# Kernel optimization log

Measured on AMD Instinct MI355X. Metric: run time of the kernel, lower is better.

## Reference

```python
import jax, jax.numpy as jnp
import numpy as np

EPS = 1e-6

def rmsnorm(x, w):
    v = jnp.mean(jnp.square(x), axis=-1, keepdims=True)
    return x * jax.lax.rsqrt(v + EPS) * w

def setup_inputs() -> dict:
    key = jax.random.key(0)
    ks = jax.random.split(key, 12)
    H, Di, L = 2048, 4096, 1024   # hidden, mamba inner (expand*H), seq tokens
    DT, N, K = 128, 16, 4         # dt_rank, d_state, d_conv
    F = 8192                      # MLP intermediate
    s = lambda k, shp, sc: jax.random.normal(k, shp, jnp.float32) * sc
    return dict(
        hidden_states=s(ks[0], (L, H), 1.0),
        in_ln_w=jnp.ones((H,), jnp.float32),
        pre_ff_ln_w=jnp.ones((H,), jnp.float32),
        in_proj_w=s(ks[1], (2 * Di, H), 0.02),
        conv_w=s(ks[2], (Di, K), 0.1),
        conv_b=s(ks[3], (Di,), 0.1),
        x_proj_w=s(ks[4], (DT + 2 * N, Di), 0.02),
        dt_ln_w=jnp.ones((DT,), jnp.float32),
        b_ln_w=jnp.ones((N,), jnp.float32),
        c_ln_w=jnp.ones((N,), jnp.float32),
        dt_proj_w=s(ks[5], (Di, DT), 0.02),
        dt_proj_b=s(ks[6], (Di,), 0.1),
        A=-jnp.exp(jax.random.uniform(ks[7], (Di, N), jnp.float32, -4.0, 0.0)),
        D=jnp.ones((Di,), jnp.float32),
        out_proj_w=s(ks[8], (H, Di), 0.02),
        gate_up_w=s(ks[9], (2 * F, H), 0.02),
        down_w=s(ks[10], (H, F), 0.02),
    )

def reference(hidden_states, in_ln_w, pre_ff_ln_w, in_proj_w, conv_w, conv_b,
              x_proj_w, dt_ln_w, b_ln_w, c_ln_w, dt_proj_w, dt_proj_b,
              A, D, out_proj_w, gate_up_w, down_w):
    residual = hidden_states
    x = rmsnorm(hidden_states, in_ln_w)
    # --- Mamba mixer (prefill / selective_scan path) ---
    proj = x @ in_proj_w.T                          # [L, 2*Di]
    Di = in_proj_w.shape[0] // 2
    h, gate = proj[:, :Di], proj[:, Di:]
    # causal depthwise conv1d, kernel K, left pad K-1, then silu
    K = conv_w.shape[1]
    L = h.shape[0]
    hp = jnp.pad(h, ((K - 1, 0), (0, 0)))           # [L+K-1, Di]
    idx = jnp.arange(L)[:, None] + jnp.arange(K)[None, :]
    h = jnp.einsum('lkd,dk->ld', hp[idx], conv_w) + conv_b
    h = jax.nn.silu(h)
    # ssm parameters
    ssm = h @ x_proj_w.T                            # [L, DT+2N]
    DTr = dt_ln_w.shape[0]
    N = b_ln_w.shape[0]
    dt = rmsnorm(ssm[:, :DTr], dt_ln_w)
    B = rmsnorm(ssm[:, DTr:DTr + N], b_ln_w)
    C = rmsnorm(ssm[:, DTr + N:], c_ln_w)
    delta = jax.nn.softplus(dt @ dt_proj_w.T + dt_proj_b)   # [L, Di]
    # selective scan (discretize then linear recurrence over L)
    dA = jnp.exp(delta[:, :, None] * A[None, :, :])         # [L, Di, N]
    dBu = delta[:, :, None] * B[:, None, :] * h[:, :, None] # [L, Di, N]
    def step(s, inp):
        da, dbu = inp
        s = da * s + dbu
        return s, s
    s0 = jnp.zeros((Di, N), jnp.float32)
    _, states = jax.lax.scan(step, s0, (dA, dBu))           # [L, Di, N]
    y = jnp.einsum('ldn,ln->ld', states, C) + h * D
    y = y * jax.nn.silu(gate)
    mixer_out = y @ out_proj_w.T                    # [L, H]
    # --- residual + pre-FF norm + gated MLP ---
    residual = residual + mixer_out
    x = rmsnorm(residual, pre_ff_ln_w)
    gu = x @ gate_up_w.T                            # [L, 2F]
    F = down_w.shape[1]
    x = jax.nn.silu(gu[:, :F]) * gu[:, F:]
    ff = x @ down_w.T
    return residual + ff
```

## Files before the change

kernel.cpp:

```cpp
#include <hip/hip_runtime.h>
#include <math.h>

typedef unsigned short u16;
typedef __bf16 bf16x8 __attribute__((ext_vector_type(8)));
typedef short s16x8 __attribute__((ext_vector_type(8)));
typedef short s16x4 __attribute__((ext_vector_type(4)));
typedef float f32x4 __attribute__((ext_vector_type(4)));

__device__ __forceinline__ u16 f2bf(float f) {
  union { float f; unsigned u; } v; v.f = f;
  unsigned u = v.u;
  unsigned r = u + 0x7fffu + ((u >> 16) & 1u);
  return (u16)(r >> 16);
}
__device__ __forceinline__ float bf2f(u16 h) {
  union { unsigned u; float f; } v; v.u = ((unsigned)h) << 16;
  return v.f;
}
__device__ __forceinline__ float fast_softplus(float x) {
  return (x > 20.f) ? x : __logf(1.f + __expf(x));
}
__device__ __forceinline__ float fast_sig(float x) {
  return __builtin_amdgcn_rcpf(1.f + __expf(-x));
}

__device__ __forceinline__ void gld_lds16(const u16* g, u16* l) {
  __builtin_amdgcn_global_load_lds(
      (const __attribute__((address_space(1))) unsigned int*)g,
      (__attribute__((address_space(3))) unsigned int*)l, 16, 0, 0);
}

__global__ __launch_bounds__(256)
void f32_to_bf16_k(const float* __restrict__ src, u16* __restrict__ dst,
                   int n, int n_valid) {
  int i = (blockIdx.x * 256 + threadIdx.x) * 4;
  if (i >= n) return;
  s16x4 o;
  if (i + 3 < n_valid) {
    float4 v = *(const float4*)(src + i);
    o[0] = (short)f2bf(v.x); o[1] = (short)f2bf(v.y);
    o[2] = (short)f2bf(v.z); o[3] = (short)f2bf(v.w);
  } else {
    o[0] = 0; o[1] = 0; o[2] = 0; o[3] = 0;
  }
  *(s16x4*)(dst + i) = o;
}

template <int BN, int MODE>
__global__ __launch_bounds__(256)
void gemm2(const u16* __restrict__ A, const u16* __restrict__ B,
           float* __restrict__ C, u16* __restrict__ Cb,
           const u16* __restrict__ aux, int M, int Nc, int K) {
  constexpr int NJ = BN / 32;
  constexpr int BISS = BN / 32;
  __shared__ __align__(16) u16 As[64 * 64];
  __shared__ __align__(16) u16 Bs[BN * 64];
  const int tid = threadIdx.x;
  const int tm0 = blockIdx.y * 64;
  const int tn0 = blockIdx.x * BN;
  const int wave = tid >> 6;
  const int lane = tid & 63;
  const int wm = (wave >> 1) * 32;
  const int wn = (wave & 1) * (BN / 2);
  const int frow = lane & 15;
  const int fc = lane >> 4;
  const int rmask = frow & 7;

  const int r0 = tid >> 3;
  const int csw = (((tid & 7) ^ (r0 & 7)) << 3);
  const u16* gA = A + (size_t)(tm0 + r0) * K + csw;
  const u16* gB = B + (size_t)(tn0 + r0) * K + csw;
  u16* lA = &As[tid * 8];
  u16* lB = &Bs[tid * 8];

  f32x4 acc[2][NJ];
  f32x4 zero = {0.f, 0.f, 0.f, 0.f};
#pragma unroll
  for (int i = 0; i < 2; ++i)
#pragma unroll
    for (int j = 0; j < NJ; ++j) acc[i][j] = zero;

  for (int kt = 0; kt < K; kt += 64) {
    __syncthreads();
    gld_lds16(gA, lA);
    gld_lds16(gA + (size_t)32 * K, lA + 2048);
#pragma unroll
    for (int b = 0; b < BISS; ++b)
      gld_lds16(gB + (size_t)32 * b * K, lB + b * 2048);
    gA += 64; gB += 64;
    __syncthreads();
#pragma unroll
    for (int s = 0; s < 2; ++s) {
      bf16x8 af[2], bfr[NJ];
#pragma unroll
      for (int i = 0; i < 2; ++i) {
        int addr = (wm + i * 16 + frow) * 64 + (((s * 4 + fc) ^ rmask) << 3);
        af[i] = __builtin_bit_cast(bf16x8, *(const s16x8*)&As[addr]);
      }
#pragma unroll
      for (int j = 0; j < NJ; ++j) {
        int addr = (wn + j * 16 + frow) * 64 + (((s * 4 + fc) ^ rmask) << 3);
        bfr[j] = __builtin_bit_cast(bf16x8, *(const s16x8*)&Bs[addr]);
      }
#pragma unroll
      for (int i = 0; i < 2; ++i)
#pragma unroll
        for (int j = 0; j < NJ; ++j)
          acc[i][j] = __builtin_amdgcn_mfma_f32_16x16x32_bf16(af[i], bfr[j], acc[i][j], 0, 0, 0);
    }
  }
  const int ccol = lane & 15;
  const int crow = (lane >> 4) * 4;
#pragma unroll
  for (int i = 0; i < 2; ++i) {
#pragma unroll
    for (int j = 0; j < NJ; ++j) {
      int gn = tn0 + wn + j * 16 + ccol;
      if (gn < Nc) {
        size_t base = (size_t)(tm0 + wm + i * 16 + crow) * Nc + gn;
#pragma unroll
        for (int r = 0; r < 4; ++r) {
          float c = acc[i][j][r];
          size_t idx = base + (size_t)r * Nc;
          if (MODE == 0) {
            C[idx] = c;
          } else if (MODE == 1) {
            Cb[idx] = f2bf(c * fast_sig(c));
          } else {
            Cb[idx] = f2bf(c * bf2f(aux[idx]));
          }
        }
      }
    }
  }
}

__device__ inline float block_reduce_sum_256(float v) {
  __shared__ float red[4];
  int lane = threadIdx.x & 63, wave = threadIdx.x >> 6;
#pragma unroll
  for (int m = 32; m > 0; m >>= 1) v += __shfl_xor(v, m, 64);
  if (lane == 0) red[wave] = v;
  __syncthreads();
  return red[0] + red[1] + red[2] + red[3];
}

__global__ __launch_bounds__(256)
void rmsnorm2048_k(const float* __restrict__ x, const float* __restrict__ w,
                   u16* __restrict__ y) {
  const int C = 2048;
  const int row = blockIdx.x;
  const int t = threadIdx.x;
  const float4* xr = (const float4*)(x + (size_t)row * C);
  float4 v0 = xr[t];
  float4 v1 = xr[t + 256];
  float ss = v0.x * v0.x + v0.y * v0.y + v0.z * v0.z + v0.w * v0.w +
             v1.x * v1.x + v1.y * v1.y + v1.z * v1.z + v1.w * v1.w;
  float tot = block_reduce_sum_256(ss);
  float sc = rsqrtf(tot * (1.0f / C) + 1e-6f);
  const float4* wr = (const float4*)w;
  float4 w0 = wr[t], w1 = wr[t + 256];
  u16* yr = y + (size_t)row * C;
  s16x4 o0, o1;
  o0[0] = (short)f2bf(v0.x * sc * w0.x); o0[1] = (short)f2bf(v0.y * sc * w0.y);
  o0[2] = (short)f2bf(v0.z * sc * w0.z); o0[3] = (short)f2bf(v0.w * sc * w0.w);
  o1[0] = (short)f2bf(v1.x * sc * w1.x); o1[1] = (short)f2bf(v1.y * sc * w1.y);
  o1[2] = (short)f2bf(v1.z * sc * w1.z); o1[3] = (short)f2bf(v1.w * sc * w1.w);
  *(s16x4*)(yr + t * 4) = o0;
  *(s16x4*)(yr + 1024 + t * 4) = o1;
}

__global__ __launch_bounds__(256)
void add_rmsnorm_k(const float* __restrict__ a, const float* __restrict__ b,
                   const float* __restrict__ w, float* __restrict__ resid,
                   u16* __restrict__ y) {
  const int C = 2048;
  const int row = blockIdx.x;
  const int t = threadIdx.x;
  const float4* ar = (const float4*)(a + (size_t)row * C);
  const float4* br = (const float4*)(b + (size_t)row * C);
  float4 v0 = ar[t], v1 = ar[t + 256];
  float4 u0 = br[t], u1 = br[t + 256];
  v0.x += u0.x; v0.y += u0.y; v0.z += u0.z; v0.w += u0.w;
  v1.x += u1.x; v1.y += u1.y; v1.z += u1.z; v1.w += u1.w;
  float4* rr = (float4*)(resid + (size_t)row * C);
  rr[t] = v0; rr[t + 256] = v1;
  float ss = v0.x * v0.x + v0.y * v0.y + v0.z * v0.z + v0.w * v0.w +
             v1.x * v1.x + v1.y * v1.y + v1.z * v1.z + v1.w * v1.w;
  float tot = block_reduce_sum_256(ss);
  float sc = rsqrtf(tot * (1.0f / C) + 1e-6f);
  const float4* wr = (const float4*)w;
  float4 w0 = wr[t], w1 = wr[t + 256];
  u16* yr = y + (size_t)row * C;
  s16x4 o0, o1;
  o0[0] = (short)f2bf(v0.x * sc * w0.x); o0[1] = (short)f2bf(v0.y * sc * w0.y);
  o0[2] = (short)f2bf(v0.z * sc * w0.z); o0[3] = (short)f2bf(v0.w * sc * w0.w);
  o1[0] = (short)f2bf(v1.x * sc * w1.x); o1[1] = (short)f2bf(v1.y * sc * w1.y);
  o1[2] = (short)f2bf(v1.z * sc * w1.z); o1[3] = (short)f2bf(v1.w * sc * w1.w);
  *(s16x4*)(yr + t * 4) = o0;
  *(s16x4*)(yr + 1024 + t * 4) = o1;
}

__global__ __launch_bounds__(256)
void conv_silu_k(const float* __restrict__ proj, const float* __restrict__ cw,
                 const float* __restrict__ cb, u16* __restrict__ h) {
  const int Di = 4096, LD = 8192;
  int idx = blockIdx.x * 256 + threadIdx.x;
  int d = idx & (Di - 1);
  int l = idx >> 12;
  float4 w = *(const float4*)(cw + (size_t)d * 4);
  float acc = cb[d];
  int ls0 = l - 3;
  if (ls0 >= 0) acc += proj[(size_t)ls0 * LD + d] * w.x;
  if (ls0 + 1 >= 0) acc += proj[(size_t)(ls0 + 1) * LD + d] * w.y;
  if (ls0 + 2 >= 0) acc += proj[(size_t)(ls0 + 2) * LD + d] * w.z;
  acc += proj[(size_t)l * LD + d] * w.w;
  h[idx] = f2bf(acc * fast_sig(acc));
}

__global__ __launch_bounds__(64)
void ssm_norm_k(const float* __restrict__ ssm, const float* __restrict__ dtw,
                const float* __restrict__ bw, const float* __restrict__ cw,
                u16* __restrict__ dtn, float* __restrict__ Bn,
                float* __restrict__ Cn) {
  int l = blockIdx.x;
  int lane = threadIdx.x;
  const float* r = ssm + (size_t)l * 160;
  float d0 = r[lane];
  float d1 = r[lane + 64];
  float bv = (lane < 16) ? r[128 + lane] : 0.f;
  float cv = (lane < 16) ? r[144 + lane] : 0.f;
  float sd = d0 * d0 + d1 * d1;
  float sb = bv * bv;
  float sc = cv * cv;
#pragma unroll
  for (int m = 32; m > 0; m >>= 1) {
    sd += __shfl_xor(sd, m, 64);
    sb += __shfl_xor(sb, m, 64);
    sc += __shfl_xor(sc, m, 64);
  }
  float scd = rsqrtf(sd * (1.f / 128.f) + 1e-6f);
  float scb = rsqrtf(sb * (1.f / 16.f) + 1e-6f);
  float scc = rsqrtf(sc * (1.f / 16.f) + 1e-6f);
  dtn[(size_t)l * 128 + lane] = f2bf(d0 * scd * dtw[lane]);
  dtn[(size_t)l * 128 + lane + 64] = f2bf(d1 * scd * dtw[lane + 64]);
  if (lane < 16) {
    Bn[(size_t)l * 16 + lane] = bv * scb * bw[lane];
    Cn[(size_t)l * 16 + lane] = cv * scc * cw[lane];
  }
}

#define NCH 32
#define CHL 32

__global__ __launch_bounds__(256)
void scan_p1(const float* __restrict__ dpre, const float* __restrict__ dtb,
             const u16* __restrict__ h, const float* __restrict__ Bn,
             const float* __restrict__ Amat,
             float* __restrict__ carryA, float* __restrict__ carryS) {
  const int Di = 4096;
  int chunk = blockIdx.x & (NCH - 1);
  int d = (blockIdx.x >> 5) * 256 + threadIdx.x;
  __shared__ float Bs[CHL * 16];
  for (int i = threadIdx.x; i < CHL * 16; i += 256)
    Bs[i] = Bn[(size_t)chunk * CHL * 16 + i];
  __syncthreads();
  float a[16];
#pragma unroll
  for (int q = 0; q < 4; ++q)
    *(float4*)&a[q * 4] = *(const float4*)(Amat + (size_t)d * 16 + q * 4);
  float bias = dtb[d];
  float s[16];
#pragma unroll
  for (int n = 0; n < 16; ++n) s[n] = 0.f;
  float sumdel = 0.f;
  int l0 = chunk * CHL;
#pragma unroll 4
  for (int j = 0; j < CHL; ++j) {
    int l = l0 + j;
    float del = fast_softplus(dpre[(size_t)l * Di + d] + bias);
    float hv = bf2f(h[(size_t)l * Di + d]);
    sumdel += del;
    float c = del * hv;
#pragma unroll
    for (int n = 0; n < 16; ++n) {
      float dA = __expf(del * a[n]);
      s[n] = dA * s[n] + c * Bs[j * 16 + n];
    }
  }
  size_t base = (size_t)chunk * 65536 + (size_t)d * 16;
#pragma unroll
  for (int n = 0; n < 16; ++n) {
    carryA[base + n] = __expf(sumdel * a[n]);
    carryS[base + n] = s[n];
  }
}

__global__ __launch_bounds__(256)
void scan_p2(const float* __restrict__ carryA, float* __restrict__ carryS) {
  int p = blockIdx.x * 256 + threadIdx.x;
  float cin = 0.f;
#pragma unroll
  for (int c = 0; c < NCH; ++c) {
    float av = carryA[(size_t)c * 65536 + p];
    float sv = carryS[(size_t)c * 65536 + p];
    float nx = av * cin + sv;
    carryS[(size_t)c * 65536 + p] = cin;
    cin = nx;
  }
}

__global__ __launch_bounds__(256)
void scan_p3(const float* __restrict__ dpre, const float* __restrict__ dtb,
             const u16* __restrict__ h, const float* __restrict__ Bn,
             const float* __restrict__ Cn, const float* __restrict__ Amat,
             const float* __restrict__ Dw, const float* __restrict__ proj,
             const float* __restrict__ carryS, u16* __restrict__ y) {
  const int Di = 4096;
  int chunk = blockIdx.x & (NCH - 1);
  int d = (blockIdx.x >> 5) * 256 + threadIdx.x;
  __shared__ float Bs[CHL * 16];
  __shared__ float Cs[CHL * 16];
  for (int i = threadIdx.x; i < CHL * 16; i += 256) {
    Bs[i] = Bn[(size_t)chunk * CHL * 16 + i];
    Cs[i] = Cn[(size_t)chunk * CHL * 16 + i];
  }
  __syncthreads();
  float a[16];
#pragma unroll
  for (int q = 0; q < 4; ++q)
    *(float4*)&a[q * 4] = *(const float4*)(Amat + (size_t)d * 16 + q * 4);
  float bias = dtb[d];
  float Dd = Dw[d];
  float s[16];
  size_t base = (size_t)chunk * 65536 + (size_t)d * 16;
#pragma unroll
  for (int q = 0; q < 4; ++q)
    *(float4*)&s[q * 4] = *(const float4*)(carryS + base + q * 4);
  int l0 = chunk * CHL;
#pragma unroll 2
  for (int j = 0; j < CHL; ++j) {
    int l = l0 + j;
    float del = fast_softplus(dpre[(size_t)l * Di + d] + bias);
    float hv = bf2f(h[(size_t)l * Di + d]);
    float c = del * hv;
    float p = 0.f;
#pragma unroll
    for (int n = 0; n < 16; ++n) {
      float dA = __expf(del * a[n]);
      s[n] = dA * s[n] + c * Bs[j * 16 + n];
      p += s[n] * Cs[j * 16 + n];
    }
    float g = proj[(size_t)l * 8192 + 4096 + d];
    float yv = p + hv * Dd;
    y[(size_t)l * Di + d] = f2bf(yv * g * fast_sig(g));
  }
}

__global__ __launch_bounds__(256)
void add_k(float* __restrict__ out, const float* __restrict__ ff) {
  int i = blockIdx.x * 256 + threadIdx.x;
  float4 a = ((const float4*)out)[i];
  float4 b = ((const float4*)ff)[i];
  a.x += b.x; a.y += b.y; a.z += b.z; a.w += b.w;
  ((float4*)out)[i] = a;
}

extern "C" void kernel_launch(void* const* d_in, const int* in_sizes, int n_in,
                              void* d_out, int out_size, void* d_ws, size_t ws_size,
                              hipStream_t stream) {
  const float* hidden      = (const float*)d_in[0];
  const float* in_ln_w     = (const float*)d_in[1];
  const float* pre_ff_ln_w = (const float*)d_in[2];
  const float* in_proj_w   = (const float*)d_in[3];
  const float* conv_w      = (const float*)d_in[4];
  const float* conv_b      = (const float*)d_in[5];
  const float* x_proj_w    = (const float*)d_in[6];
  const float* dt_ln_w     = (const float*)d_in[7];
  const float* b_ln_w      = (const float*)d_in[8];
  const float* c_ln_w      = (const float*)d_in[9];
  const float* dt_proj_w   = (const float*)d_in[10];
  const float* dt_proj_b   = (const float*)d_in[11];
  const float* Amat        = (const float*)d_in[12];
  const float* Dw          = (const float*)d_in[13];
  const float* out_proj_w  = (const float*)d_in[14];
  const float* gate_up_w   = (const float*)d_in[15];
  const float* down_w      = (const float*)d_in[16];
  float* out = (float*)d_out;
  float* ws = (float*)d_ws;

  const int L = 1024, H = 2048, Di = 4096, F = 8192;

  u16*   wbuf   = (u16*)ws;
  float* carryA = ws + 2097152;
  float* carryS = ws + 4194304;
  float* proj   = ws + 8388608;
  float* dpre   = ws + 16777216;
  u16*   hbuf   = (u16*)(ws + 20971520);
  u16*   xnorm  = (u16*)(ws + 23068672);
  float* ssm    = ws + 24117248;
  u16*   dtn    = (u16*)(ws + 24281088);
  float* Bn     = ws + 24346624;
  float* Cn     = ws + 24363008;
  u16*   ybuf   = (u16*)(ws + 24379392);
  float* mix    = ws + 16777216;
  u16*   x2     = (u16*)(ws + 18874368);
  u16*   sg     = (u16*)(ws + 8388608);
  u16*   x3     = (u16*)(ws + 12582912);
  float* ff     = ws + 19922944;

  rmsnorm2048_k<<<L, 256, 0, stream>>>(hidden, in_ln_w, xnorm);
  f32_to_bf16_k<<<16384, 256, 0, stream>>>(in_proj_w, wbuf, 16777216, 16777216);
  gemm2<128, 0><<<dim3(64, 16), 256, 0, stream>>>(xnorm, wbuf, proj, nullptr, nullptr, L, 8192, 2048);
  conv_silu_k<<<(L * Di) / 256, 256, 0, stream>>>(proj, conv_w, conv_b, hbuf);
  f32_to_bf16_k<<<1024, 256, 0, stream>>>(x_proj_w, wbuf, 1048576, 655360);
  gemm2<64, 0><<<dim3(4, 16), 256, 0, stream>>>(hbuf, wbuf, ssm, nullptr, nullptr, L, 160, 4096);
  ssm_norm_k<<<L, 64, 0, stream>>>(ssm, dt_ln_w, b_ln_w, c_ln_w, dtn, Bn, Cn);
  f32_to_bf16_k<<<512, 256, 0, stream>>>(dt_proj_w, wbuf, 524288, 524288);
  gemm2<128, 0><<<dim3(32, 16), 256, 0, stream>>>(dtn, wbuf, dpre, nullptr, nullptr, L, 4096, 128);
  scan_p1<<<16 * NCH, 256, 0, stream>>>(dpre, dt_proj_b, hbuf, Bn, Amat, carryA, carryS);
  scan_p2<<<256, 256, 0, stream>>>(carryA, carryS);
  scan_p3<<<16 * NCH, 256, 0, stream>>>(dpre, dt_proj_b, hbuf, Bn, Cn, Amat, Dw, proj, carryS, ybuf);
  f32_to_bf16_k<<<8192, 256, 0, stream>>>(out_proj_w, wbuf, 8388608, 8388608);
  gemm2<64, 0><<<dim3(32, 16), 256, 0, stream>>>(ybuf, wbuf, mix, nullptr, nullptr, L, 2048, 4096);
  add_rmsnorm_k<<<L, 256, 0, stream>>>(hidden, mix, pre_ff_ln_w, out, x2);
  f32_to_bf16_k<<<16384, 256, 0, stream>>>(gate_up_w, wbuf, 16777216, 16777216);
  gemm2<128, 1><<<dim3(64, 16), 256, 0, stream>>>(x2, wbuf, nullptr, sg, nullptr, L, 8192, 2048);
  f32_to_bf16_k<<<16384, 256, 0, stream>>>(gate_up_w + 16777216, wbuf, 16777216, 16777216);
  gemm2<128, 2><<<dim3(64, 16), 256, 0, stream>>>(x2, wbuf, nullptr, x3, sg, L, 8192, 2048);
  f32_to_bf16_k<<<16384, 256, 0, stream>>>(down_w, wbuf, 16777216, 16777216);
  gemm2<64, 0><<<dim3(32, 16), 256, 0, stream>>>(x3, wbuf, ff, nullptr, nullptr, L, 2048, 8192);
  add_k<<<(L * H / 4) / 256, 256, 0, stream>>>(out, ff);
}
```

Before: 730.2 us.

## Use 128x128 GEMM tiles and split-K for the narrow output projections

Adds a gemm128 kernel in which each of four waves computes a 64x64 sub-tile, giving more data reuse per block than the older gemm2. It replaces the large GEMMs with it. The out_proj and down projections (N=2048) get a 4-way split-K over grid z, and the partial sums are reduced inside the following add+rmsnorm and residual-add kernels. This keeps the GPU occupied despite fewer output tiles, but writes and reads four fp32 partial buffers and raises register pressure.

Result: faster. 685.2 us (-6.2%).

```diff
diff --git a/kernel.cpp b/kernel.cpp
--- a/kernel.cpp
+++ b/kernel.cpp
@@ -129,6 +129,94 @@
           } else {
             Cb[idx] = f2bf(c * bf2f(aux[idx]));
           }
+        }
+      }
+    }
+  }
+}
+
+template <int MODE, int SPLITK>
+__global__ __launch_bounds__(256)
+void gemm128(const u16* __restrict__ A, const u16* __restrict__ B,
+             float* __restrict__ C, u16* __restrict__ Cb,
+             const u16* __restrict__ aux, int M, int Nc, int K) {
+  __shared__ __align__(16) u16 As[128 * 64];
+  __shared__ __align__(16) u16 Bs[128 * 64];
+  const int tid = threadIdx.x;
+  const int tm0 = blockIdx.y * 128;
+  const int tn0 = blockIdx.x * 128;
+  const int kslice = K / SPLITK;
+  const int k0 = blockIdx.z * kslice;
+  const int wave = tid >> 6;
+  const int lane = tid & 63;
+  const int wm = (wave >> 1) * 64;
+  const int wn = (wave & 1) * 64;
+  const int frow = lane & 15;
+  const int fc = lane >> 4;
+  const int rmask = frow & 7;
+
+  const int r0 = tid >> 3;
+  const int csw = (((tid & 7) ^ (r0 & 7)) << 3);
+  const u16* gA = A + (size_t)(tm0 + r0) * K + k0 + csw;
+  const u16* gB = B + (size_t)(tn0 + r0) * K + k0 + csw;
+  u16* lA = &As[tid * 8];
+  u16* lB = &Bs[tid * 8];
+
+  f32x4 acc[4][4];
+  f32x4 zero = {0.f, 0.f, 0.f, 0.f};
+#pragma unroll
+  for (int i = 0; i < 4; ++i)
+#pragma unroll
+    for (int j = 0; j < 4; ++j) acc[i][j] = zero;
+
+  for (int kt = 0; kt < kslice; kt += 64) {
+    __syncthreads();
+#pragma unroll
+    for (int b = 0; b < 4; ++b) {
+      gld_lds16(gA + (size_t)(32 * b) * K, lA + b * 2048);
+      gld_lds16(gB + (size_t)(32 * b) * K, lB + b * 2048);
+    }
+    gA += 64; gB += 64;
+    __syncthreads();
+#pragma unroll
+    for (int s = 0; s < 2; ++s) {
+      bf16x8 af[4], bfr[4];
+#pragma unroll
+      for (int i = 0; i < 4; ++i) {
+        int addr = (wm + i * 16 + frow) * 64 + (((s * 4 + fc) ^ rmask) << 3);
+        af[i] = __builtin_bit_cast(bf16x8, *(const s16x8*)&As[addr]);
+      }
+#pragma unroll
+      for (int j = 0; j < 4; ++j) {
+        int addr = (wn + j * 16 + frow) * 64 + (((s * 4 + fc) ^ rmask) << 3);
+        bfr[j] = __builtin_bit_cast(bf16x8, *(const s16x8*)&Bs[addr]);
+      }
+#pragma unroll
+      for (int i = 0; i < 4; ++i)
+#pragma unroll
+        for (int j = 0; j < 4; ++j)
+          acc[i][j] = __builtin_amdgcn_mfma_f32_16x16x32_bf16(af[i], bfr[j], acc[i][j], 0, 0, 0);
+    }
+  }
+  const int ccol = lane & 15;
+  const int crow = (lane >> 4) * 4;
+  float* Cp = C + (size_t)blockIdx.z * ((size_t)M * Nc);
+#pragma unroll
+  for (int i = 0; i < 4; ++i) {
+#pragma unroll
+    for (int j = 0; j < 4; ++j) {
+      int gn = tn0 + wn + j * 16 + ccol;
+      size_t base = (size_t)(tm0 + wm + i * 16 + crow) * Nc + gn;
+#pragma unroll
+      for (int r = 0; r < 4; ++r) {
+        float c = acc[i][j][r];
+        size_t idx = base + (size_t)r * Nc;
+        if (MODE == 0) {
+          Cp[idx] = c;
+        } else if (MODE == 1) {
+          Cb[idx] = f2bf(c * fast_sig(c));
+        } else {
+          Cb[idx] = f2bf(c * bf2f(aux[idx]));
         }
       }
     }
@@ -171,18 +259,22 @@
 }
 
 __global__ __launch_bounds__(256)
-void add_rmsnorm_k(const float* __restrict__ a, const float* __restrict__ b,
-                   const float* __restrict__ w, float* __restrict__ resid,
-                   u16* __restrict__ y) {
+void add_rmsnorm4_k(const float* __restrict__ a, const float* __restrict__ p,
+                    const float* __restrict__ w, float* __restrict__ resid,
+                    u16* __restrict__ y) {
   const int C = 2048;
+  const size_t S = (size_t)1024 * 2048;
   const int row = blockIdx.x;
   const int t = threadIdx.x;
   const float4* ar = (const float4*)(a + (size_t)row * C);
-  const float4* br = (const float4*)(b + (size_t)row * C);
   float4 v0 = ar[t], v1 = ar[t + 256];
-  float4 u0 = br[t], u1 = br[t + 256];
-  v0.x += u0.x; v0.y += u0.y; v0.z += u0.z; v0.w += u0.w;
-  v1.x += u1.x; v1.y += u1.y; v1.z += u1.z; v1.w += u1.w;
+#pragma unroll
+  for (int s = 0; s < 4; ++s) {
+    const float4* br = (const float4*)(p + s * S + (size_t)row * C);
+    float4 u0 = br[t], u1 = br[t + 256];
+    v0.x += u0.x; v0.y += u0.y; v0.z += u0.z; v0.w += u0.w;
+    v1.x += u1.x; v1.y += u1.y; v1.z += u1.z; v1.w += u1.w;
+  }
   float4* rr = (float4*)(resid + (size_t)row * C);
   rr[t] = v0; rr[t + 256] = v1;
   float ss = v0.x * v0.x + v0.y * v0.y + v0.z * v0.z + v0.w * v0.w +
@@ -358,11 +450,15 @@
 }
 
 __global__ __launch_bounds__(256)
-void add_k(float* __restrict__ out, const float* __restrict__ ff) {
+void add4_k(float* __restrict__ out, const float* __restrict__ p) {
+  const size_t S = (size_t)1024 * 2048;
   int i = blockIdx.x * 256 + threadIdx.x;
   float4 a = ((const float4*)out)[i];
-  float4 b = ((const float4*)ff)[i];
-  a.x += b.x; a.y += b.y; a.z += b.z; a.w += b.w;
+#pragma unroll
+  for (int s = 0; s < 4; ++s) {
+    float4 b = ((const float4*)(p + s * S))[i];
+    a.x += b.x; a.y += b.y; a.z += b.z; a.w += b.w;
+  }
   ((float4*)out)[i] = a;
 }
 
@@ -403,15 +499,15 @@
   float* Bn     = ws + 24346624;
   float* Cn     = ws + 24363008;
   u16*   ybuf   = (u16*)(ws + 24379392);
-  float* mix    = ws + 16777216;
+  float* mixp   = ws + 8388608;
   u16*   x2     = (u16*)(ws + 18874368);
   u16*   sg     = (u16*)(ws + 8388608);
   u16*   x3     = (u16*)(ws + 12582912);
-  float* ff     = ws + 19922944;
+  float* ffp    = ws + 16777216;
 
   rmsnorm2048_k<<<L, 256, 0, stream>>>(hidden, in_ln_w, xnorm);
   f32_to_bf16_k<<<16384, 256, 0, stream>>>(in_proj_w, wbuf, 16777216, 16777216);
-  gemm2<128, 0><<<dim3(64, 16), 256, 0, stream>>>(xnorm, wbuf, proj, nullptr, nullptr, L, 8192, 2048);
+  gemm128<0, 1><<<dim3(64, 8), 256, 0, stream>>>(xnorm, wbuf, proj, nullptr, nullptr, L, 8192, 2048);
   conv_silu_k<<<(L * Di) / 256, 256, 0, stream>>>(proj, conv_w, conv_b, hbuf);
   f32_to_bf16_k<<<1024, 256, 0, stream>>>(x_proj_w, wbuf, 1048576, 655360);
   gemm2<64, 0><<<dim3(4, 16), 256, 0, stream>>>(hbuf, wbuf, ssm, nullptr, nullptr, L, 160, 4096);
@@ -422,13 +518,13 @@
   scan_p2<<<256, 256, 0, stream>>>(carryA, carryS);
   scan_p3<<<16 * NCH, 256, 0, stream>>>(dpre, dt_proj_b, hbuf, Bn, Cn, Amat, Dw, proj, carryS, ybuf);
   f32_to_bf16_k<<<8192, 256, 0, stream>>>(out_proj_w, wbuf, 8388608, 8388608);
-  gemm2<64, 0><<<dim3(32, 16), 256, 0, stream>>>(ybuf, wbuf, mix, nullptr, nullptr, L, 2048, 4096);
-  add_rmsnorm_k<<<L, 256, 0, stream>>>(hidden, mix, pre_ff_ln_w, out, x2);
+  gemm128<0, 4><<<dim3(16, 8, 4), 256, 0, stream>>>(ybuf, wbuf, mixp, nullptr, nullptr, L, 2048, 4096);
+  add_rmsnorm4_k<<<L, 256, 0, stream>>>(hidden, mixp, pre_ff_ln_w, out, x2);
   f32_to_bf16_k<<<16384, 256, 0, stream>>>(gate_up_w, wbuf, 16777216, 16777216);
-  gemm2<128, 1><<<dim3(64, 16), 256, 0, stream>>>(x2, wbuf, nullptr, sg, nullptr, L, 8192, 2048);
+  gemm128<1, 1><<<dim3(64, 8), 256, 0, stream>>>(x2, wbuf, nullptr, sg, nullptr, L, 8192, 2048);
   f32_to_bf16_k<<<16384, 256, 0, stream>>>(gate_up_w + 16777216, wbuf, 16777216, 16777216);
-  gemm2<128, 2><<<dim3(64, 16), 256, 0, stream>>>(x2, wbuf, nullptr, x3, sg, L, 8192, 2048);
+  gemm128<2, 1><<<dim3(64, 8), 256, 0, stream>>>(x2, wbuf, nullptr, x3, sg, L, 8192, 2048);
   f32_to_bf16_k<<<16384, 256, 0, stream>>>(down_w, wbuf, 16777216, 16777216);
-  gemm2<64, 0><<<dim3(32, 16), 256, 0, stream>>>(x3, wbuf, ff, nullptr, nullptr, L, 2048, 8192);
-  add_k<<<(L * H / 4) / 256, 256, 0, stream>>>(out, ff);
-}
+  gemm128<0, 4><<<dim3(16, 8, 4), 256, 0, stream>>>(x3, wbuf, ffp, nullptr, nullptr, L, 2048, 8192);
+  add4_k<<<(L * H / 4) / 256, 256, 0, stream>>>(out, ffp);
+}
```
